# Kernel tuning notes

Hardware: AMD Instinct MI355X
Metric: run time of the kernel (lower is better)

Reference implementation:

```python
import jax, jax.numpy as jnp
import numpy as np

DIM = 256; QK = 256; HEADS = 8; TOPK = 2; WV = 2; WH = 2
SCALE = QK ** -0.5


def setup_inputs() -> dict:
    key = jax.random.key(0)
    ks = jax.random.split(key, 6)
    x = jax.random.normal(ks[0], (4, DIM, 64, 64), jnp.float32)
    Wqkv = jax.random.normal(ks[1], (DIM, 2 * QK + DIM), jnp.float32) * 0.02
    bqkv = jnp.zeros((2 * QK + DIM,), jnp.float32)
    Wo = jax.random.normal(ks[2], (DIM, DIM), jnp.float32) * 0.02
    bo = jnp.zeros((DIM,), jnp.float32)
    lepe_w = jax.random.normal(ks[3], (3, 3, 1, DIM), jnp.float32) * 0.1  # HWIO depthwise
    lepe_b = jnp.zeros((DIM,), jnp.float32)
    return {"x": x, "Wqkv": Wqkv, "bqkv": bqkv, "Wo": Wo, "bo": bo,
            "lepe_w": lepe_w, "lepe_b": lepe_b}


def _dwconv(x, w, b):
    # depthwise 3x3 conv, NHWC
    y = jax.lax.conv_general_dilated(x, w, (1, 1), 'SAME',
                                     dimension_numbers=('NHWC', 'HWIO', 'NHWC'),
                                     feature_group_count=x.shape[-1])
    return y + b


def _branch(win, Wqkv, bqkv, lepe_w, lepe_b, to_image):
    n, p2, h, w, _ = win.shape
    w2 = h * w
    qkv = win @ Wqkv + bqkv
    q = qkv[..., :QK]
    kv = qkv[..., QK:]                                  # [n,p2,h,w,QK+DIM]
    q_pix = q.reshape(n, p2, w2, QK)
    kv_pix = kv.reshape(n, p2, w2, QK + DIM)            # identity kv_down
    # region routing (detached in original)
    q_win = jax.lax.stop_gradient(q).mean((2, 3))       # [n,p2,QK]
    k_win = jax.lax.stop_gradient(kv[..., :QK]).mean((2, 3))
    logit = jnp.einsum('npc,nqc->npq', q_win * SCALE, k_win)
    _, r_idx = jax.lax.top_k(logit, TOPK)               # [n,p2,TOPK]
    # gather selected KV windows (mul_weight='none')
    kv_sel = jax.vmap(lambda kvb, idxb: kvb[idxb])(kv_pix, r_idx)  # [n,p2,k,w2,ckv]
    k_sel = kv_sel[..., :QK].reshape(n, p2, TOPK * w2, HEADS, QK // HEADS)
    v_sel = kv_sel[..., QK:].reshape(n, p2, TOPK * w2, HEADS, DIM // HEADS)
    qh = q_pix.reshape(n, p2, w2, HEADS, QK // HEADS)
    attn = jax.nn.softmax(jnp.einsum('npqhd,npkhd->nphqk', qh * SCALE, k_sel), axis=-1)
    out = jnp.einsum('nphqk,npkhd->npqhd', attn, v_sel).reshape(n, p2, h, w, DIM)
    lepe = _dwconv(to_image(kv[..., QK:]), lepe_w, lepe_b)
    return to_image(out) + lepe


def reference(x, Wqkv, bqkv, Wo, bo, lepe_w, lepe_b):
    xh = x.transpose(0, 2, 3, 1)                        # NHWC
    N, H, W, C = xh.shape
    v_win, h_win = H // WV, W // WH
    # vertical branch: horizontal strips of height WV, full width
    vm = xh.reshape(N, v_win, WV, W, C)
    # horizontal branch: vertical strips of width WH, full height
    hm = xh.reshape(N, H, h_win, WH, C).transpose(0, 2, 1, 3, 4)
    img_v = lambda a: a.reshape(N, H, W, a.shape[-1])
    img_h = lambda a: a.transpose(0, 2, 1, 3, 4).reshape(N, H, W, a.shape[-1])
    o1 = _branch(vm, Wqkv, bqkv, lepe_w, lepe_b, img_v)
    o2 = _branch(hm, Wqkv, bqkv, lepe_w, lepe_b, img_h)
    out = (o1 @ Wo + bo) + (o2 @ Wo + bo)
    return out.transpose(0, 3, 1, 2)                    # back to NCHW
```

## Files before the change

### kernel.cpp

```cpp
#include <hip/hip_runtime.h>
#include <hip/hip_bf16.h>
#include <math.h>

#define NBATCH 4
#define HW     4096
#define NPIX   16384
#define SCALE  0.0625f
#define QLOG2E (0.0625f * 1.44269504088896340736f)

typedef __attribute__((ext_vector_type(8))) short bf16x8;
typedef __attribute__((ext_vector_type(4))) float f32x4;

__device__ __forceinline__ int pixmap(int b, int n, int p, int pos){
  return (b == 0) ? (n*HW + p*128 + pos)
                  : (n*HW + (pos >> 1)*64 + (p << 1) + (pos & 1));
}

__device__ __forceinline__ ushort f2b(float x){
  __hip_bfloat16 h = __float2bfloat16(x);
  return *reinterpret_cast<ushort*>(&h);
}
__device__ __forceinline__ float b2f(ushort u){
  __hip_bfloat16 h = *reinterpret_cast<__hip_bfloat16*>(&u);
  return __bfloat162float(h);
}
__device__ __forceinline__ uint pk2t(float a, float b){
  return (__float_as_uint(a) >> 16) | (__float_as_uint(b) & 0xFFFF0000u);
}

__global__ __launch_bounds__(256) void k_xt(
    const float* __restrict__ x, ushort* __restrict__ Xb)
{
  __shared__ float T[32][257];
  const int n = blockIdx.y, hw0 = blockIdx.x * 32;
  const int tid = threadIdx.x;
  const int hl = tid & 31, cg = tid >> 5;
  #pragma unroll 8
  for(int i = 0; i < 32; i++){
    const int c = i*8 + cg;
    T[hl][c] = x[((size_t)(n*256 + c))*4096 + hw0 + hl];
  }
  __syncthreads();
  const int c0 = (tid & 31)*8, pb = tid >> 5;
  #pragma unroll
  for(int i = 0; i < 4; i++){
    const int p = pb + 8*i;
    union { bf16x8 v; ushort u[8]; } U;
    #pragma unroll
    for(int j = 0; j < 8; j++) U.u[j] = f2b(T[p][c0 + j]);
    *(bf16x8*)(Xb + ((size_t)(n*HW + hw0 + p))*256 + c0) = U.v;
  }
}

__global__ __launch_bounds__(256) void k_wprep(
    const float* __restrict__ Wqkv, const float* __restrict__ Wo,
    ushort* __restrict__ Wt, ushort* __restrict__ WoT)
{
  const int o = blockIdx.x, t = threadIdx.x;
  if(o < 768){
    Wt[(size_t)o*256 + t] = f2b(Wqkv[(size_t)t*768 + o]);
  } else {
    const int c = o - 768;
    WoT[(size_t)c*256 + t] = f2b(Wo[(size_t)t*256 + c]);
  }
}

__global__ __launch_bounds__(256) void k_qkv_mfma(
    const ushort* __restrict__ Xb, const ushort* __restrict__ Wt,
    const float* __restrict__ bqkv, ushort* __restrict__ QKVb,
    ushort* __restrict__ Vt)
{
  const int tid = threadIdx.x;
  const int l = tid & 63, w = tid >> 6;
  const int wr = w >> 1, wc = w & 1;
  const int q16 = l & 15, g = l >> 4;
  const int row0 = blockIdx.x*128 + wr*64;
  const int col0 = blockIdx.y*128 + wc*64;

  f32x4 acc[4][4];
  #pragma unroll
  for(int i = 0; i < 4; i++)
    #pragma unroll
    for(int j = 0; j < 4; j++) acc[i][j] = (f32x4){0,0,0,0};

  const ushort* Ab = Xb + (size_t)(row0 + q16)*256 + 8*g;
  const ushort* Bb = Wt + (size_t)(col0 + q16)*256 + 8*g;

  #pragma unroll
  for(int ks = 0; ks < 8; ks++){
    const int k0 = ks*32;
    bf16x8 a[4], b[4];
    #pragma unroll
    for(int i = 0; i < 4; i++) a[i] = *(const bf16x8*)(Ab + (size_t)(16*i)*256 + k0);
    #pragma unroll
    for(int j = 0; j < 4; j++) b[j] = *(const bf16x8*)(Bb + (size_t)(16*j)*256 + k0);
    #pragma unroll
    for(int i = 0; i < 4; i++)
      #pragma unroll
      for(int j = 0; j < 4; j++)
        acc[i][j] = __builtin_amdgcn_mfma_f32_16x16x32_bf16(a[i], b[j], acc[i][j], 0, 0, 0);
  }

  const int n = row0 >> 12, hwb = row0 & 4095;
  #pragma unroll
  for(int j = 0; j < 4; j++){
    const int col = col0 + 16*j + q16;
    const float bias = bqkv[col];
    const float sc = (col < 256) ? QLOG2E : 1.f;
    #pragma unroll
    for(int i = 0; i < 4; i++){
      ushort4 u;
      u.x = f2b((acc[i][j][0] + bias) * sc);
      u.y = f2b((acc[i][j][1] + bias) * sc);
      u.z = f2b((acc[i][j][2] + bias) * sc);
      u.w = f2b((acc[i][j][3] + bias) * sc);
      const int row = row0 + 16*i + 4*g;
      QKVb[(size_t)(row+0)*768 + col] = u.x;
      QKVb[(size_t)(row+1)*768 + col] = u.y;
      QKVb[(size_t)(row+2)*768 + col] = u.z;
      QKVb[(size_t)(row+3)*768 + col] = u.w;
      if(col >= 512){
        *(ushort4*)&Vt[((size_t)(n*256 + col - 512))*4096 + hwb + 16*i + 4*g] = u;
      }
    }
  }
}

__global__ __launch_bounds__(256) void k_xmean(
    const float* __restrict__ x, float* __restrict__ xwin)
{
  const int n = blockIdx.y;
  const int c = blockIdx.x*4 + (threadIdx.x >> 6);
  const int l = threadIdx.x & 63;
  const float* xc = x + ((size_t)(n*256 + c))*4096;

  float4 cs[8];
  #pragma unroll
  for(int i = 0; i < 8; i++) cs[i] = (float4){0,0,0,0};
  float rsum = 0.f;
  const float4* xr = (const float4*)(xc + l*64);
  #pragma unroll
  for(int i = 0; i < 16; i++){
    const float4 v = xr[i];
    rsum += (v.x+v.y)+(v.z+v.w);
    const float p0 = v.x+v.y, p1 = v.z+v.w;
    if(i & 1){ cs[i>>1].z += p0; cs[i>>1].w += p1; }
    else     { cs[i>>1].x += p0; cs[i>>1].y += p1; }
  }
  #pragma unroll
  for(int i = 0; i < 8; i++){
    #pragma unroll
    for(int sb = 0; sb < 6; sb++){
      const int s = 1 << sb;
      cs[i].x += __shfl_xor(cs[i].x, s);
      cs[i].y += __shfl_xor(cs[i].y, s);
      cs[i].z += __shfl_xor(cs[i].z, s);
      cs[i].w += __shfl_xor(cs[i].w, s);
    }
  }
  const int p = l & 31;
  const float rp = __shfl(rsum, 2*p) + __shfl(rsum, 2*p + 1);
  float cp;
  {
    const int hi = p >> 2, lo = p & 3;
    const float4 q = hi==0?cs[0]:hi==1?cs[1]:hi==2?cs[2]:hi==3?cs[3]
                   : hi==4?cs[4]:hi==5?cs[5]:hi==6?cs[6]:cs[7];
    cp = lo==0?q.x : lo==1?q.y : lo==2?q.z : q.w;
  }
  if(l < 32){
    xwin[((size_t)((0*NBATCH + n)*32 + p))*256 + c] = rp * (1.f/128.f);
    xwin[((size_t)((1*NBATCH + n)*32 + p))*256 + c] = cp * (1.f/128.f);
  }
}

__global__ __launch_bounds__(256) void k_win_gemm(
    const float* __restrict__ xwin, const float* __restrict__ Wqkv,
    const float* __restrict__ bqkv, float* __restrict__ qwin, float* __restrict__ kwin)
{
  __shared__ float xs[256];
  const int row = blockIdx.x;
  const int tid = threadIdx.x;
  xs[tid] = xwin[(size_t)row*256 + tid];
  __syncthreads();
  #pragma unroll
  for(int half = 0; half < 2; half++){
    const int col = half*256 + tid;
    float s = 0.f;
    for(int k = 0; k < 256; k++) s += xs[k] * Wqkv[(size_t)k*768 + col];
    s += bqkv[col];
    if(half == 0) qwin[(size_t)row*256 + tid] = s;
    else          kwin[(size_t)row*256 + tid] = s;
  }
}

__global__ __launch_bounds__(256) void k_logits_top2(
    const float* __restrict__ qwin, const float* __restrict__ kwin, int* __restrict__ ridx)
{
  const int n = blockIdx.x, b = blockIdx.y;
  __shared__ float lg[32][32];
  const int base = ((b*NBATCH + n)*32)*256;
  for(int t = threadIdx.x; t < 1024; t += 256){
    const int p = t >> 5, q = t & 31;
    const float* qp = qwin + base + p*256;
    const float* kq = kwin + base + q*256;
    float s = 0.f;
    for(int c = 0; c < 256; c++) s += qp[c]*kq[c];
    lg[p][q] = s * SCALE;
  }
  __syncthreads();
  if(threadIdx.x < 32){
    const int p = threadIdx.x;
    float m0 = -INFINITY; int i0 = 0;
    for(int q = 0; q < 32; q++){ const float v = lg[p][q]; if(v > m0){ m0 = v; i0 = q; } }
    float m1 = -INFINITY; int i1 = 0;
    for(int q = 0; q < 32; q++){ if(q == i0) continue; const float v = lg[p][q]; if(v > m1){ m1 = v; i1 = q; } }
    const int o = ((b*NBATCH + n)*32 + p)*2;
    ridx[o] = i0; ridx[o+1] = i1;
  }
}

struct KVFrag { bf16x8 kf0, kf1, vf0, vf1; };

__device__ __forceinline__ KVFrag load_kv(
    const ushort* __restrict__ QKVb, const ushort* __restrict__ Vt,
    int b, int n, int wsel, int posb, int hd, int q16, int g)
{
  KVFrag f;
  const int kp0 = pixmap(b, n, wsel, posb + q16);
  f.kf0 = *(const bf16x8*)(QKVb + (size_t)kp0*768 + 256 + hd*32 + 8*g);
  const int kp1 = pixmap(b, n, wsel, posb + 16 + q16);
  f.kf1 = *(const bf16x8*)(QKVb + (size_t)kp1*768 + 256 + hd*32 + 8*g);
  if(b == 0){
    const ushort* base = Vt + ((size_t)(n*256 + hd*32 + q16))*4096 + wsel*128 + posb + 4*g;
    union { bf16x8 v; ushort4 h[2]; } U0, U1;
    U0.h[0] = *(const ushort4*)(base);
    U0.h[1] = *(const ushort4*)(base + 16);
    U1.h[0] = *(const ushort4*)(base + (size_t)16*4096);
    U1.h[1] = *(const ushort4*)(base + (size_t)16*4096 + 16);
    f.vf0 = U0.v; f.vf1 = U1.v;
  } else {
    const int h0 = (posb + 4*g) >> 1;
    const ushort* base = Vt + ((size_t)(n*256 + hd*32 + q16))*4096 + 2*wsel;
    union { bf16x8 v; uint u[4]; } U0, U1;
    U0.u[0] = *(const uint*)(base + (h0    )*64);
    U0.u[1] = *(const uint*)(base + (h0 + 1)*64);
    U0.u[2] = *(const uint*)(base + (h0 + 8)*64);
    U0.u[3] = *(const uint*)(base + (h0 + 9)*64);
    const ushort* base1 = base + (size_t)16*4096;
    U1.u[0] = *(const uint*)(base1 + (h0    )*64);
    U1.u[1] = *(const uint*)(base1 + (h0 + 1)*64);
    U1.u[2] = *(const uint*)(base1 + (h0 + 8)*64);
    U1.u[3] = *(const uint*)(base1 + (h0 + 9)*64);
    f.vf0 = U0.v; f.vf1 = U1.v;
  }
  return f;
}

__global__ __launch_bounds__(256) void k_attn_mfma(
    const ushort* __restrict__ QKVb, const ushort* __restrict__ Vt,
    const int* __restrict__ ridx, ushort* __restrict__ Ob)
{
  int id = blockIdx.x*4 + (threadIdx.x >> 6);
  const int hd = id & 7;  id >>= 3;
  const int p  = id & 31; id >>= 5;
  const int n  = id & 3;  id >>= 2;
  const int b  = id;
  const int l = threadIdx.x & 63;
  const int q16 = l & 15, g = l >> 4;

  const int ro = ((b*NBATCH + n)*32 + p)*2;
  const int r0 = ridx[ro], r1 = ridx[ro+1];

  int qpix[8];
  bf16x8 qf[8];
  #pragma unroll
  for(int m = 0; m < 8; m++){
    qpix[m] = pixmap(b, n, p, m*16 + q16);
    qf[m] = *(const bf16x8*)(QKVb + (size_t)qpix[m]*768 + hd*32 + 8*g);
  }

  f32x4 acc0[8], acc1[8];
  float rs[8];
  #pragma unroll
  for(int m = 0; m < 8; m++){
    acc0[m] = (f32x4){0,0,0,0}; acc1[m] = (f32x4){0,0,0,0}; rs[m] = 0.f;
  }

  #define COMPUTE(F)                                                            \
    __builtin_amdgcn_s_setprio(1);                                              \
    _Pragma("unroll")                                                           \
    for(int m = 0; m < 8; m++){                                                 \
      const f32x4 z = {0,0,0,0};                                                \
      f32x4 s0 = __builtin_amdgcn_mfma_f32_16x16x32_bf16((F).kf0, qf[m], z, 0, 0, 0); \
      f32x4 s1 = __builtin_amdgcn_mfma_f32_16x16x32_bf16((F).kf1, qf[m], z, 0, 0, 0); \
      const float e00 = exp2f(s0[0]), e01 = exp2f(s0[1]), e02 = exp2f(s0[2]), e03 = exp2f(s0[3]); \
      const float e10 = exp2f(s1[0]), e11 = exp2f(s1[1]), e12 = exp2f(s1[2]), e13 = exp2f(s1[3]); \
      rs[m] += ((e00+e01)+(e02+e03)) + ((e10+e11)+(e12+e13));                   \
      union { bf16x8 v; uint u[4]; } P;                                         \
      P.u[0] = pk2t(e00, e01);                                                  \
      P.u[1] = pk2t(e02, e03);                                                  \
      P.u[2] = pk2t(e10, e11);                                                  \
      P.u[3] = pk2t(e12, e13);                                                  \
      acc0[m] = __builtin_amdgcn_mfma_f32_16x16x32_bf16((F).vf0, P.v, acc0[m], 0, 0, 0); \
      acc1[m] = __builtin_amdgcn_mfma_f32_16x16x32_bf16((F).vf1, P.v, acc1[m], 0, 0, 0); \
    }                                                                           \
    __builtin_amdgcn_s_setprio(0);

  KVFrag fA = load_kv(QKVb, Vt, b, n, r0, 0, hd, q16, g);
  for(int cc = 0; cc < 8; cc += 2){
    const int w1 = (cc+1 < 4) ? r0 : r1;
    KVFrag fB = load_kv(QKVb, Vt, b, n, w1, (32*(cc+1)) & 127, hd, q16, g);
    COMPUTE(fA);
    if(cc + 2 < 8){
      const int w2 = (cc+2 < 4) ? r0 : r1;
      fA = load_kv(QKVb, Vt, b, n, w2, (32*(cc+2)) & 127, hd, q16, g);
    }
    COMPUTE(fB);
  }
  #undef COMPUTE

  #pragma unroll
  for(int m = 0; m < 8; m++){
    float r = rs[m];
    r += __shfl_xor(r, 16);
    r += __shfl_xor(r, 32);
    rs[m] = 1.f / r;
  }
  #pragma unroll
  for(int m = 0; m < 8; m++){
    ushort* op = Ob + ((size_t)b*NPIX + qpix[m])*256 + hd*32 + 4*g;
    const float iv = rs[m];
    ushort4 o0 = { f2b(acc0[m][0]*iv), f2b(acc0[m][1]*iv), f2b(acc0[m][2]*iv), f2b(acc0[m][3]*iv) };
    ushort4 o1 = { f2b(acc1[m][0]*iv), f2b(acc1[m][1]*iv), f2b(acc1[m][2]*iv), f2b(acc1[m][3]*iv) };
    *(ushort4*)op = o0;
    *(ushort4*)(op + 16) = o1;
  }
}

__global__ __launch_bounds__(256) void k_combine_lepe(
    const ushort* __restrict__ QKVb, const ushort* __restrict__ Ob0,
    const ushort* __restrict__ Ob1,
    const float* __restrict__ lw, const float* __restrict__ lb, ushort* __restrict__ Sb)
{
  const int pix = blockIdx.x;
  const int c = threadIdx.x;
  const int n = pix >> 12, rem = pix & 4095;
  const int h = rem >> 6, w = rem & 63;
  float conv = 0.f;
  #pragma unroll
  for(int kh = 0; kh < 3; kh++){
    const int hh = h + kh - 1;
    if(hh < 0 || hh >= 64) continue;
    #pragma unroll
    for(int kw = 0; kw < 3; kw++){
      const int wi = w + kw - 1;
      if(wi < 0 || wi >= 64) continue;
      const int np = (n*64 + hh)*64 + wi;
      conv += b2f(QKVb[(size_t)np*768 + 512 + c]) * lw[(kh*3 + kw)*256 + c];
    }
  }
  const size_t idx = (size_t)pix*256 + c;
  Sb[idx] = f2b(b2f(Ob0[idx]) + b2f(Ob1[idx]) + 2.f*(conv + lb[c]));
}

__global__ __launch_bounds__(256) void k_out_mfma(
    const ushort* __restrict__ Sb, const ushort* __restrict__ WoT,
    const float* __restrict__ bo, float* __restrict__ out)
{
  const int tid = threadIdx.x;
  const int l = tid & 63, w = tid >> 6;
  const int wr = w >> 1, wc = w & 1;
  const int q16 = l & 15, g = l >> 4;
  const int c0   = blockIdx.x*128 + wr*64;
  const int pix0 = blockIdx.y*128 + wc*64;
  const int n = pix0 >> 12, rem0 = pix0 & 4095;

  f32x4 acc[4][4];
  #pragma unroll
  for(int i = 0; i < 4; i++)
    #pragma unroll
    for(int j = 0; j < 4; j++) acc[i][j] = (f32x4){0,0,0,0};

  const ushort* Ab = WoT + (size_t)(c0 + q16)*256 + 8*g;
  const ushort* Bb = Sb  + (size_t)(pix0 + q16)*256 + 8*g;

  #pragma unroll
  for(int ks = 0; ks < 8; ks++){
    const int k0 = ks*32;
    bf16x8 a[4], b[4];
    #pragma unroll
    for(int i = 0; i < 4; i++) a[i] = *(const bf16x8*)(Ab + (size_t)(16*i)*256 + k0);
    #pragma unroll
    for(int j = 0; j < 4; j++) b[j] = *(const bf16x8*)(Bb + (size_t)(16*j)*256 + k0);
    #pragma unroll
    for(int i = 0; i < 4; i++)
      #pragma unroll
      for(int j = 0; j < 4; j++)
        acc[i][j] = __builtin_amdgcn_mfma_f32_16x16x32_bf16(a[i], b[j], acc[i][j], 0, 0, 0);
  }

  float* outn = out + (size_t)n*256*4096;
  #pragma unroll
  for(int i = 0; i < 4; i++){
    #pragma unroll
    for(int r = 0; r < 4; r++){
      const int c = c0 + 16*i + 4*g + r;
      const float bias = 2.f*bo[c];
      #pragma unroll
      for(int j = 0; j < 4; j++){
        const int rem = rem0 + 16*j + q16;
        outn[(size_t)c*4096 + rem] = acc[i][j][r] + bias;
      }
    }
  }
}

extern "C" void kernel_launch(void* const* d_in, const int* in_sizes, int n_in,
                              void* d_out, int out_size, void* d_ws, size_t ws_size,
                              hipStream_t stream)
{
  const float* x    = (const float*)d_in[0];
  const float* Wqkv = (const float*)d_in[1];
  const float* bqkv = (const float*)d_in[2];
  const float* Wo   = (const float*)d_in[3];
  const float* bo   = (const float*)d_in[4];
  const float* lw   = (const float*)d_in[5];
  const float* lb   = (const float*)d_in[6];
  float* out = (float*)d_out;

  char* w = (char*)d_ws;
  ushort* Xb   = (ushort*)w; w += (size_t)NPIX*256*2;
  ushort* Wt   = (ushort*)w; w += (size_t)768*256*2;
  ushort* WoT  = (ushort*)w; w += (size_t)256*256*2;
  ushort* QKVb = (ushort*)w; w += (size_t)NPIX*768*2;
  ushort* Vt   = (ushort*)w; w += (size_t)NPIX*256*2;
  ushort* Ob   = (ushort*)w; w += (size_t)2*NPIX*256*2;
  ushort* Sb   = (ushort*)w; w += (size_t)NPIX*256*2;
  float*  xwin = (float*)w;  w += (size_t)2*NBATCH*32*256*4;
  float*  qwin = (float*)w;  w += (size_t)2*NBATCH*32*256*4;
  float*  kwin = (float*)w;  w += (size_t)2*NBATCH*32*256*4;
  int*    ridx = (int*)w;    w += (size_t)2*NBATCH*32*2*4;

  ushort* Ob0 = Ob;
  ushort* Ob1 = Ob + (size_t)NPIX*256;

  k_xt          <<<dim3(128,NBATCH), 256, 0, stream>>>(x, Xb);
  k_wprep       <<<1024, 256, 0, stream>>>(Wqkv, Wo, Wt, WoT);
  k_qkv_mfma    <<<dim3(128,6), 256, 0, stream>>>(Xb, Wt, bqkv, QKVb, Vt);
  k_xmean       <<<dim3(64,NBATCH), 256, 0, stream>>>(x, xwin);
  k_win_gemm    <<<256, 256, 0, stream>>>(xwin, Wqkv, bqkv, qwin, kwin);
  k_logits_top2 <<<dim3(NBATCH,2), 256, 0, stream>>>(qwin, kwin, ridx);
  k_attn_mfma   <<<512, 256, 0, stream>>>(QKVb, Vt, ridx, Ob);
  k_combine_lepe<<<NPIX, 256, 0, stream>>>(QKVb, Ob0, Ob1, lw, lb, Sb);
  k_out_mfma    <<<dim3(2,128), 256, 0, stream>>>(Sb, WoT, bo, out);
}
```

Measured before the change: 182.3 us.

## Split QKV buffer into head-major Q/K and row-major V layouts

```diff
diff --git a/kernel.cpp b/kernel.cpp
--- a/kernel.cpp
+++ b/kernel.cpp
@@ -11,9 +11,9 @@
 typedef __attribute__((ext_vector_type(8))) short bf16x8;
 typedef __attribute__((ext_vector_type(4))) float f32x4;
 
-__device__ __forceinline__ int pixmap(int b, int n, int p, int pos){
-  return (b == 0) ? (n*HW + p*128 + pos)
-                  : (n*HW + (pos >> 1)*64 + (p << 1) + (pos & 1));
+__device__ __forceinline__ int hwloc(int b, int p, int pos){
+  return (b == 0) ? (p*128 + pos)
+                  : ((pos >> 1)*64 + (p << 1) + (pos & 1));
 }
 
 __device__ __forceinline__ ushort f2b(float x){
@@ -67,8 +67,8 @@
 
 __global__ __launch_bounds__(256) void k_qkv_mfma(
     const ushort* __restrict__ Xb, const ushort* __restrict__ Wt,
-    const float* __restrict__ bqkv, ushort* __restrict__ QKVb,
-    ushort* __restrict__ Vt)
+    const float* __restrict__ bqkv, ushort* __restrict__ Qh,
+    ushort* __restrict__ Kh, ushort* __restrict__ Vrow, ushort* __restrict__ Vt)
 {
   const int tid = threadIdx.x;
   const int l = tid & 63, w = tid >> 6;
@@ -114,13 +114,22 @@
       u.y = f2b((acc[i][j][1] + bias) * sc);
       u.z = f2b((acc[i][j][2] + bias) * sc);
       u.w = f2b((acc[i][j][3] + bias) * sc);
-      const int row = row0 + 16*i + 4*g;
-      QKVb[(size_t)(row+0)*768 + col] = u.x;
-      QKVb[(size_t)(row+1)*768 + col] = u.y;
-      QKVb[(size_t)(row+2)*768 + col] = u.z;
-      QKVb[(size_t)(row+3)*768 + col] = u.w;
-      if(col >= 512){
-        *(ushort4*)&Vt[((size_t)(n*256 + col - 512))*4096 + hwb + 16*i + 4*g] = u;
+      const int hw = hwb + 16*i + 4*g;
+      if(col < 256){
+        ushort* Q = Qh + ((size_t)(n*8 + (col >> 5))*4096 + hw)*32 + (col & 31);
+        Q[0] = u.x; Q[32] = u.y; Q[64] = u.z; Q[96] = u.w;
+      } else if(col < 512){
+        const int cc = col - 256;
+        ushort* K = Kh + ((size_t)(n*8 + (cc >> 5))*4096 + hw)*32 + (cc & 31);
+        K[0] = u.x; K[32] = u.y; K[64] = u.z; K[96] = u.w;
+      } else {
+        const int cc = col - 512;
+        const int row = row0 + 16*i + 4*g;
+        Vrow[(size_t)(row+0)*256 + cc] = u.x;
+        Vrow[(size_t)(row+1)*256 + cc] = u.y;
+        Vrow[(size_t)(row+2)*256 + cc] = u.z;
+        Vrow[(size_t)(row+3)*256 + cc] = u.w;
+        *(ushort4*)&Vt[((size_t)(n*256 + cc))*4096 + hw] = u;
       }
     }
   }
@@ -222,14 +231,14 @@
 struct KVFrag { bf16x8 kf0, kf1, vf0, vf1; };
 
 __device__ __forceinline__ KVFrag load_kv(
-    const ushort* __restrict__ QKVb, const ushort* __restrict__ Vt,
-    int b, int n, int wsel, int posb, int hd, int q16, int g)
+    const ushort* __restrict__ Kh, const ushort* __restrict__ Vt,
+    int b, int n, int nh8, int wsel, int posb, int hd, int q16, int g)
 {
   KVFrag f;
-  const int kp0 = pixmap(b, n, wsel, posb + q16);
-  f.kf0 = *(const bf16x8*)(QKVb + (size_t)kp0*768 + 256 + hd*32 + 8*g);
-  const int kp1 = pixmap(b, n, wsel, posb + 16 + q16);
-  f.kf1 = *(const bf16x8*)(QKVb + (size_t)kp1*768 + 256 + hd*32 + 8*g);
+  const int hk0 = hwloc(b, wsel, posb + q16);
+  f.kf0 = *(const bf16x8*)(Kh + ((size_t)nh8*4096 + hk0)*32 + 8*g);
+  const int hk1 = hwloc(b, wsel, posb + 16 + q16);
+  f.kf1 = *(const bf16x8*)(Kh + ((size_t)nh8*4096 + hk1)*32 + 8*g);
   if(b == 0){
     const ushort* base = Vt + ((size_t)(n*256 + hd*32 + q16))*4096 + wsel*128 + posb + 4*g;
     union { bf16x8 v; ushort4 h[2]; } U0, U1;
@@ -257,8 +266,9 @@
 }
 
 __global__ __launch_bounds__(256) void k_attn_mfma(
-    const ushort* __restrict__ QKVb, const ushort* __restrict__ Vt,
-    const int* __restrict__ ridx, ushort* __restrict__ Ob)
+    const ushort* __restrict__ Qh, const ushort* __restrict__ Kh,
+    const ushort* __restrict__ Vt, const int* __restrict__ ridx,
+    ushort* __restrict__ Ob)
 {
   int id = blockIdx.x*4 + (threadIdx.x >> 6);
   const int hd = id & 7;  id >>= 3;
@@ -267,16 +277,17 @@
   const int b  = id;
   const int l = threadIdx.x & 63;
   const int q16 = l & 15, g = l >> 4;
+  const int nh8 = n*8 + hd;
 
   const int ro = ((b*NBATCH + n)*32 + p)*2;
   const int r0 = ridx[ro], r1 = ridx[ro+1];
 
-  int qpix[8];
+  int qhw[8];
   bf16x8 qf[8];
   #pragma unroll
   for(int m = 0; m < 8; m++){
-    qpix[m] = pixmap(b, n, p, m*16 + q16);
-    qf[m] = *(const bf16x8*)(QKVb + (size_t)qpix[m]*768 + hd*32 + 8*g);
+    qhw[m] = hwloc(b, p, m*16 + q16);
+    qf[m] = *(const bf16x8*)(Qh + ((size_t)nh8*4096 + qhw[m])*32 + 8*g);
   }
 
   f32x4 acc0[8], acc1[8];
@@ -306,14 +317,14 @@
     }                                                                           \
     __builtin_amdgcn_s_setprio(0);
 
-  KVFrag fA = load_kv(QKVb, Vt, b, n, r0, 0, hd, q16, g);
+  KVFrag fA = load_kv(Kh, Vt, b, n, nh8, r0, 0, hd, q16, g);
   for(int cc = 0; cc < 8; cc += 2){
     const int w1 = (cc+1 < 4) ? r0 : r1;
-    KVFrag fB = load_kv(QKVb, Vt, b, n, w1, (32*(cc+1)) & 127, hd, q16, g);
+    KVFrag fB = load_kv(Kh, Vt, b, n, nh8, w1, (32*(cc+1)) & 127, hd, q16, g);
     COMPUTE(fA);
     if(cc + 2 < 8){
       const int w2 = (cc+2 < 4) ? r0 : r1;
-      fA = load_kv(QKVb, Vt, b, n, w2, (32*(cc+2)) & 127, hd, q16, g);
+      fA = load_kv(Kh, Vt, b, n, nh8, w2, (32*(cc+2)) & 127, hd, q16, g);
     }
     COMPUTE(fB);
   }
@@ -328,7 +339,7 @@
   }
   #pragma unroll
   for(int m = 0; m < 8; m++){
-    ushort* op = Ob + ((size_t)b*NPIX + qpix[m])*256 + hd*32 + 4*g;
+    ushort* op = Ob + ((size_t)b*NPIX + n*4096 + qhw[m])*256 + hd*32 + 4*g;
     const float iv = rs[m];
     ushort4 o0 = { f2b(acc0[m][0]*iv), f2b(acc0[m][1]*iv), f2b(acc0[m][2]*iv), f2b(acc0[m][3]*iv) };
     ushort4 o1 = { f2b(acc1[m][0]*iv), f2b(acc1[m][1]*iv), f2b(acc1[m][2]*iv), f2b(acc1[m][3]*iv) };
@@ -338,7 +349,7 @@
 }
 
 __global__ __launch_bounds__(256) void k_combine_lepe(
-    const ushort* __restrict__ QKVb, const ushort* __restrict__ Ob0,
+    const ushort* __restrict__ Vrow, const ushort* __restrict__ Ob0,
     const ushort* __restrict__ Ob1,
     const float* __restrict__ lw, const float* __restrict__ lb, ushort* __restrict__ Sb)
 {
@@ -356,7 +367,7 @@
       const int wi = w + kw - 1;
       if(wi < 0 || wi >= 64) continue;
       const int np = (n*64 + hh)*64 + wi;
-      conv += b2f(QKVb[(size_t)np*768 + 512 + c]) * lw[(kh*3 + kw)*256 + c];
+      conv += b2f(Vrow[(size_t)np*256 + c]) * lw[(kh*3 + kw)*256 + c];
     }
   }
   const size_t idx = (size_t)pix*256 + c;
@@ -432,7 +443,9 @@
   ushort* Xb   = (ushort*)w; w += (size_t)NPIX*256*2;
   ushort* Wt   = (ushort*)w; w += (size_t)768*256*2;
   ushort* WoT  = (ushort*)w; w += (size_t)256*256*2;
-  ushort* QKVb = (ushort*)w; w += (size_t)NPIX*768*2;
+  ushort* Qh   = (ushort*)w; w += (size_t)NPIX*256*2;
+  ushort* Kh   = (ushort*)w; w += (size_t)NPIX*256*2;
+  ushort* Vrow = (ushort*)w; w += (size_t)NPIX*256*2;
   ushort* Vt   = (ushort*)w; w += (size_t)NPIX*256*2;
   ushort* Ob   = (ushort*)w; w += (size_t)2*NPIX*256*2;
   ushort* Sb   = (ushort*)w; w += (size_t)NPIX*256*2;
@@ -446,11 +459,11 @@
 
   k_xt          <<<dim3(128,NBATCH), 256, 0, stream>>>(x, Xb);
   k_wprep       <<<1024, 256, 0, stream>>>(Wqkv, Wo, Wt, WoT);
-  k_qkv_mfma    <<<dim3(128,6), 256, 0, stream>>>(Xb, Wt, bqkv, QKVb, Vt);
+  k_qkv_mfma    <<<dim3(128,6), 256, 0, stream>>>(Xb, Wt, bqkv, Qh, Kh, Vrow, Vt);
   k_xmean       <<<dim3(64,NBATCH), 256, 0, stream>>>(x, xwin);
   k_win_gemm    <<<256, 256, 0, stream>>>(xwin, Wqkv, bqkv, qwin, kwin);
   k_logits_top2 <<<dim3(NBATCH,2), 256, 0, stream>>>(qwin, kwin, ridx);
-  k_attn_mfma   <<<512, 256, 0, stream>>>(QKVb, Vt, ridx, Ob);
-  k_combine_lepe<<<NPIX, 256, 0, stream>>>(QKVb, Ob0, Ob1, lw, lb, Sb);
+  k_attn_mfma   <<<512, 256, 0, stream>>>(Qh, Kh, Vt, ridx, Ob);
+  k_combine_lepe<<<NPIX, 256, 0, stream>>>(Vrow, Ob0, Ob1, lw, lb, Sb);
   k_out_mfma    <<<dim3(2,128), 256, 0, stream>>>(Sb, WoT, bo, out);
 }
```

New measurement: 188.6 us. +3.5%, slower.
